# Optimization experiments

Hardware: AMD Instinct MI355X
Metric: run time of the kernel (lower is better)

Reference implementation:

```python
import jax, jax.numpy as jnp
import numpy as np

B, N, P, K, D = 8, 2048, 64, 32, 384
DEPTH, DI, DS, DCONV, DTR, NC = 12, 768, 16, 4, 24, 40
BN_EPS = 1e-5


def _spread_bits(v):
    v = v & 1023
    v = (v | (v << 16)) & 50331903
    v = (v | (v << 8)) & 50393103
    v = (v | (v << 4)) & 51130563
    v = (v | (v << 2)) & 153391689
    return v


def _zkey(x, y, z):
    return _spread_bits(x) | (_spread_bits(y) << 1) | (_spread_bits(z) << 2)


def _sfc_order(xyz, trans):
    lo = xyz.min(0, keepdims=True)
    hi = xyz.max(0, keepdims=True)
    q = jnp.clip(((xyz - lo) / (hi - lo + 1e-6) * 1023.0).astype(jnp.int32), 0, 1023)
    if trans:
        keys = _zkey(q[:, 2], q[:, 1], q[:, 0])
    else:
        keys = _zkey(q[:, 0], q[:, 1], q[:, 2])
    return jnp.argsort(keys)


def _ln(x, g, b):
    m = x.mean(-1, keepdims=True)
    v = jnp.var(x, axis=-1, keepdims=True)
    return (x - m) / jnp.sqrt(v + 1e-5) * g + b


def _bn_eval(x, g, b):
    # BatchNorm in eval mode, running_mean=0 / running_var=1
    return x * (g / np.float32(np.sqrt(1.0 + BN_EPS))) + b


def _patch_embed_one(xyz, w1, b1, g1, be1, w2, b2, g2, be2, w3, b3, g3, be3):
    # xyz: (N,3)
    cidx = (jnp.arange(P) * (N / P)).astype(jnp.int32)
    centers = xyz[cidx]                                      # (P,3)
    d2 = ((centers[:, None, :] - xyz[None, :, :]) ** 2).sum(-1)  # (P,N)
    _, knn = jax.lax.top_k(-d2, K)                           # (P,K) smallest dists
    nx = xyz[knn] - centers[:, None, :]                      # (P,K,3)
    h = jax.nn.gelu(_bn_eval(nx @ w1.T + b1, g1, be1), approximate=False)   # (P,K,64)
    h = jax.nn.gelu(_bn_eval(h @ w2.T + b2, g2, be2), approximate=False)    # (P,K,128)
    h = _bn_eval(h @ w3.T + b3, g3, be3)                     # (P,K,384)
    return h.max(1), centers


def _mamba(x, in_w, conv_w, conv_b, xp_w, dt_w, dt_b, Alog, Dp, out_w):
    # x: (B,L,D)
    Bsz, L, _ = x.shape
    xz = x @ in_w.T                                          # (B,L,2*DI)
    xc, z = xz[..., :DI], xz[..., DI:]
    xpad = jnp.pad(xc, ((0, 0), (DCONV - 1, 0), (0, 0)))
    xc = sum(xpad[:, j:j + L, :] * conv_w[:, j] for j in range(DCONV)) + conv_b
    xc = jax.nn.silu(xc)
    x_dbl = xc @ xp_w.T                                      # (B,L,DTR+2*DS)
    dt = x_dbl[..., :DTR]
    Bm = x_dbl[..., DTR:DTR + DS]
    Cm = x_dbl[..., DTR + DS:]
    delta = jax.nn.softplus(dt @ dt_w.T + dt_b)              # (B,L,DI)
    A = -jnp.exp(Alog)                                       # (DI,DS)

    def step(h, inp):
        d_t, B_t, C_t, u_t = inp                             # (B,DI),(B,DS),(B,DS),(B,DI)
        h = h * jnp.exp(d_t[..., None] * A) + (d_t * u_t)[..., None] * B_t[:, None, :]
        return h, jnp.einsum('bds,bs->bd', h, C_t)

    h0 = jnp.zeros((Bsz, DI, DS), x.dtype)
    inps = (delta.transpose(1, 0, 2), Bm.transpose(1, 0, 2),
            Cm.transpose(1, 0, 2), xc.transpose(1, 0, 2))
    _, ys = jax.lax.scan(step, h0, inps)                     # (L,B,DI)
    y = ys.transpose(1, 0, 2) + Dp * xc
    y = y * jax.nn.silu(z)
    return y @ out_w.T


def setup_inputs() -> dict:
    key = jax.random.key(0)
    ks = iter(jax.random.split(key, 64))
    nrm = lambda *s: jax.random.normal(next(ks), s, jnp.float32) * 0.02
    inp = {
        'data': jax.random.normal(next(ks), (B, N, 3), jnp.float32),
        'pe_w1': nrm(64, 3), 'pe_b1': jnp.zeros(64), 'pe_g1': jnp.ones(64), 'pe_be1': jnp.zeros(64),
        'pe_w2': nrm(128, 64), 'pe_b2': jnp.zeros(128), 'pe_g2': jnp.ones(128), 'pe_be2': jnp.zeros(128),
        'pe_w3': nrm(D, 128), 'pe_b3': jnp.zeros(D), 'pe_g3': jnp.ones(D), 'pe_be3': jnp.zeros(D),
        'oi_h_scale': jnp.ones(D), 'oi_h_shift': jnp.zeros(D),
        'oi_th_scale': jnp.ones(D), 'oi_th_shift': jnp.zeros(D),
        'pos_embed': nrm(1, P, D),
        'blk_ln_g': jnp.ones((DEPTH, D)), 'blk_ln_b': jnp.zeros((DEPTH, D)),
        'blk_in_w': nrm(DEPTH, 2 * DI, D),
        'blk_conv_w': nrm(DEPTH, DI, DCONV), 'blk_conv_b': jnp.zeros((DEPTH, DI)),
        'blk_xp_w': nrm(DEPTH, DTR + 2 * DS, DI),
        'blk_dt_w': nrm(DEPTH, DI, DTR), 'blk_dt_b': jnp.full((DEPTH, DI), -4.0),
        'blk_Alog': jnp.tile(jnp.log(jnp.arange(1, DS + 1, dtype=jnp.float32)), (DEPTH, DI, 1)),
        'blk_D': jnp.ones((DEPTH, DI)),
        'blk_out_w': nrm(DEPTH, D, DI),
        'norm_g': jnp.ones(D), 'norm_b': jnp.zeros(D),
        'mlp_w1': nrm(256, D), 'mlp_b1': jnp.zeros(256),
        'mlp_w2': nrm(64, 256), 'mlp_b2': jnp.zeros(64),
        'mlp_w3': nrm(NC, 64), 'mlp_b3': jnp.zeros(NC),
    }
    return inp


def reference(data, pe_w1, pe_b1, pe_g1, pe_be1, pe_w2, pe_b2, pe_g2, pe_be2,
              pe_w3, pe_b3, pe_g3, pe_be3, oi_h_scale, oi_h_shift, oi_th_scale,
              oi_th_shift, pos_embed, blk_ln_g, blk_ln_b, blk_in_w, blk_conv_w,
              blk_conv_b, blk_xp_w, blk_dt_w, blk_dt_b, blk_Alog, blk_D,
              blk_out_w, norm_g, norm_b, mlp_w1, mlp_b1, mlp_w2, mlp_b2,
              mlp_w3, mlp_b3):
    xyz = data[:, :, :3]
    tokens, centers = jax.vmap(
        _patch_embed_one, in_axes=(0,) + (None,) * 12)(
        xyz, pe_w1, pe_b1, pe_g1, pe_be1, pe_w2, pe_b2, pe_g2, pe_be2,
        pe_w3, pe_b3, pe_g3, pe_be3)                         # (B,P,D),(B,P,3)
    order_h = jax.vmap(lambda c: _sfc_order(c, False))(centers)
    order_th = jax.vmap(lambda c: _sfc_order(c, True))(centers)
    th = jnp.take_along_axis(tokens, order_h[:, :, None], axis=1) * oi_h_scale + oi_h_shift
    tth = jnp.take_along_axis(tokens, order_th[:, :, None], axis=1) * oi_th_scale + oi_th_shift
    t = jnp.concatenate([th + pos_embed, tth + pos_embed], axis=1)  # (B,2P,D)
    for i in range(DEPTH):
        t = t + _mamba(_ln(t, blk_ln_g[i], blk_ln_b[i]),
                       blk_in_w[i], blk_conv_w[i], blk_conv_b[i], blk_xp_w[i],
                       blk_dt_w[i], blk_dt_b[i], blk_Alog[i], blk_D[i], blk_out_w[i])
    t = _ln(t, norm_g, norm_b)
    x = t.mean(1)
    x = jax.nn.relu(x @ mlp_w1.T + mlp_b1)
    x = jax.nn.relu(x @ mlp_w2.T + mlp_b2)
    return x @ mlp_w3.T + mlp_b3
```

## Files before the change

kernel.cpp:

```cpp
#include <hip/hip_runtime.h>
#include <math.h>

#define BB 8
#define NN 2048
#define PP 64
#define KK 32
#define DD 384
#define DEPTH 12
#define DI 768
#define DS 16
#define DCONV 4
#define DTR 24
#define NC 40
#define LL 128
#define XROW (DTR + 2 * DS)
#define NR (BB * LL)

using bf16x8 = __attribute__((ext_vector_type(8))) short;
using floatx4 = __attribute__((ext_vector_type(4))) float;

__device__ __forceinline__ float gelu_exact(float x) {
    return 0.5f * x * (1.0f + erff(x * 0.70710678118654752440f));
}
__device__ __forceinline__ float siluf(float x) {
    return x / (1.0f + expf(-x));
}
__device__ __forceinline__ unsigned short f2bf(float f) {
    unsigned u = __float_as_uint(f);
    u += 0x7fffu + ((u >> 16) & 1u);
    return (unsigned short)(u >> 16);
}
__device__ __forceinline__ float bf2f(short s) {
    return __uint_as_float(((unsigned)(unsigned short)s) << 16);
}
__device__ __forceinline__ unsigned spread_bits(unsigned v) {
    v &= 1023u;
    v = (v | (v << 16)) & 50331903u;
    v = (v | (v << 8)) & 50393103u;
    v = (v | (v << 4)) & 51130563u;
    v = (v | (v << 2)) & 153391689u;
    return v;
}

__global__ void k_cvt(const float* __restrict__ in_w, const float* __restrict__ out_w,
                      const float* __restrict__ pe_w3, const float* __restrict__ xp,
                      const float* __restrict__ w2,
                      unsigned short* __restrict__ inwbf, unsigned short* __restrict__ owbf,
                      unsigned short* __restrict__ w3bf, unsigned short* __restrict__ xpbf,
                      unsigned short* __restrict__ w2bf)
{
    int idx = (blockIdx.x * 256 + threadIdx.x) * 4;
    const int n1 = DEPTH * 2 * DI * DD;
    const int n2 = DEPTH * DD * DI;
    const int n3 = DD * 128;
    const int n4 = DEPTH * 64 * DI;
    const int n5 = 128 * 64;
    if (idx < n1) {
        float4 v = *(const float4*)(in_w + idx);
        ushort4 o; o.x = f2bf(v.x); o.y = f2bf(v.y); o.z = f2bf(v.z); o.w = f2bf(v.w);
        *(ushort4*)(inwbf + idx) = o;
        return;
    }
    idx -= n1;
    if (idx < n2) {
        float4 v = *(const float4*)(out_w + idx);
        ushort4 o; o.x = f2bf(v.x); o.y = f2bf(v.y); o.z = f2bf(v.z); o.w = f2bf(v.w);
        *(ushort4*)(owbf + idx) = o;
        return;
    }
    idx -= n2;
    if (idx < n3) {
        float4 v = *(const float4*)(pe_w3 + idx);
        ushort4 o; o.x = f2bf(v.x); o.y = f2bf(v.y); o.z = f2bf(v.z); o.w = f2bf(v.w);
        *(ushort4*)(w3bf + idx) = o;
        return;
    }
    idx -= n3;
    if (idx < n4) {
        int i = idx / (64 * DI);
        int rem = idx - i * 64 * DI;
        int n = rem / DI, k = rem % DI;
        ushort4 o;
        if (n < XROW) {
            float4 v = *(const float4*)(xp + (size_t)i * XROW * DI + (size_t)n * DI + k);
            o.x = f2bf(v.x); o.y = f2bf(v.y); o.z = f2bf(v.z); o.w = f2bf(v.w);
        } else {
            o.x = o.y = o.z = o.w = 0;
        }
        *(ushort4*)(xpbf + (size_t)i * 64 * DI + (size_t)n * DI + k) = o;
        return;
    }
    idx -= n4;
    if (idx < n5) {
        float4 v = *(const float4*)(w2 + idx);
        ushort4 o; o.x = f2bf(v.x); o.y = f2bf(v.y); o.z = f2bf(v.z); o.w = f2bf(v.w);
        *(ushort4*)(w2bf + idx) = o;
    }
}

__global__ __launch_bounds__(256) void k_patch(
    const float* __restrict__ data,
    const float* __restrict__ w1, const float* __restrict__ b1,
    const float* __restrict__ g1, const float* __restrict__ be1,
    const unsigned short* __restrict__ w2bf, const float* __restrict__ b2,
    const float* __restrict__ g2, const float* __restrict__ be2,
    const unsigned short* __restrict__ w3bf, const float* __restrict__ b3,
    const float* __restrict__ g3, const float* __restrict__ be3,
    float* __restrict__ tokens, float* __restrict__ centers)
{
    const int bp = blockIdx.x;
    const int b = bp >> 6, p = bp & 63;
    const int tid = threadIdx.x;
    const float* X = data + (size_t)b * NN * 3;
    const float inv_den = 0.99999500003749968752f;

    __shared__ int hist[4][4][256];
    __shared__ int klist[KK];
    __shared__ int eqlist[256];
    __shared__ int s_kth, s_byte, s_cnt, s_eqcnt;
    __shared__ float nxs[KK * 3];
    __shared__ short h1b[KK][72];
    __shared__ short h2b[KK][136];

    const float cx = X[p * 32 * 3 + 0];
    const float cy = X[p * 32 * 3 + 1];
    const float cz = X[p * 32 * 3 + 2];
    if (tid == 0) {
        centers[(b * PP + p) * 3 + 0] = cx;
        centers[(b * PP + p) * 3 + 1] = cy;
        centers[(b * PP + p) * 3 + 2] = cz;
        s_kth = KK; s_cnt = 0; s_eqcnt = 0;
    }
    for (int i = tid; i < 4 * 4 * 256; i += 256) ((int*)hist)[i] = 0;

    const int wave = tid >> 6, lane = tid & 63;

    {
        unsigned key[8];
#pragma unroll
        for (int q = 0; q < 8; q++) {
            int i = tid + 256 * q;
            float dx = cx - X[i * 3 + 0];
            float dy = cy - X[i * 3 + 1];
            float dz = cz - X[i * 3 + 2];
            float d2 = dx * dx + dy * dy + dz * dz;
            key[q] = __float_as_uint(d2);
        }
        __syncthreads();
        unsigned prefix = 0;
        for (int rnd = 3; rnd >= 0; rnd--) {
            const int sh = rnd * 8;
            const int rslot = 3 - rnd;
            const unsigned pmask = (rnd == 3) ? 0u : (0xFFFFFFFFu << (8 * (rnd + 1)));
#pragma unroll
            for (int q = 0; q < 8; q++)
                if ((key[q] & pmask) == prefix)
                    atomicAdd(&hist[rslot][wave][(key[q] >> sh) & 255], 1);
            __syncthreads();
            if (wave == 0) {
                int c[4], tot = 0;
#pragma unroll
                for (int j = 0; j < 4; j++) {
                    int s4 = 0;
#pragma unroll
                    for (int w = 0; w < 4; w++) s4 += hist[rslot][w][lane * 4 + j];
                    c[j] = s4; tot += s4;
                }
                int inc = tot;
#pragma unroll
                for (int off = 1; off < 64; off <<= 1) {
                    int u = __shfl_up(inc, off);
                    if (lane >= off) inc += u;
                }
                int exc = inc - tot;
                int kth = s_kth;
                bool has = (exc < kth) && (exc + tot >= kth);
                unsigned long long bal = __ballot(has);
                int src = __ffsll(bal) - 1;
                if (lane == src) {
                    int rem = kth - exc;
                    int j = 0, cum = 0;
                    while (cum + c[j] < rem) { cum += c[j]; j++; }
                    s_byte = lane * 4 + j;
                    s_kth = rem - cum;
                }
            }
            __syncthreads();
            prefix |= ((unsigned)s_byte) << sh;
        }
        const unsigned kstar = prefix;
        const int need = s_kth;
#pragma unroll
        for (int q = 0; q < 8; q++) {
            int i = tid + 256 * q;
            if (key[q] < kstar) {
                int pos = atomicAdd(&s_cnt, 1);
                klist[pos] = i;
            } else if (key[q] == kstar) {
                int pos = atomicAdd(&s_eqcnt, 1);
                if (pos < 256) eqlist[pos] = i;
            }
        }
        __syncthreads();
        if (tid == 0) {
            int base = s_cnt;
            int ne = s_eqcnt < 256 ? s_eqcnt : 256;
            for (int k = 0; k < need; k++) {
                int best = 0x7fffffff, bi = 0;
                for (int j = 0; j < ne; j++)
                    if (eqlist[j] < best) { best = eqlist[j]; bi = j; }
                klist[base + k] = best;
                eqlist[bi] = 0x7fffffff;
            }
        }
        __syncthreads();
    }

    if (tid < KK) {
        int q = klist[tid];
        nxs[tid * 3 + 0] = X[q * 3 + 0] - cx;
        nxs[tid * 3 + 1] = X[q * 3 + 1] - cy;
        nxs[tid * 3 + 2] = X[q * 3 + 2] - cz;
    }
    __syncthreads();

    for (int e = tid; e < KK * 64; e += 256) {
        int j = e >> 6, c = e & 63;
        float v = nxs[j * 3 + 0] * w1[c * 3 + 0] + nxs[j * 3 + 1] * w1[c * 3 + 1] +
                  nxs[j * 3 + 2] * w1[c * 3 + 2] + b1[c];
        v = v * (g1[c] * inv_den) + be1[c];
        h1b[j][c] = (short)f2bf(gelu_exact(v));
    }
    __syncthreads();

    const int quad = lane >> 4, r = lane & 15;

    {
        floatx4 acc2[2][2] = {};
#pragma unroll
        for (int ks = 0; ks < 2; ks++) {
            const int k0 = ks * 32;
            bf16x8 af[2], bfv[2];
#pragma unroll
            for (int mi = 0; mi < 2; mi++)
                af[mi] = *(const bf16x8*)&h1b[mi * 16 + r][quad * 8 + k0];
#pragma unroll
            for (int jj = 0; jj < 2; jj++) {
                int n = wave * 32 + jj * 16 + r;
                bfv[jj] = *(const bf16x8*)(w2bf + (size_t)n * 64 + quad * 8 + k0);
            }
#pragma unroll
            for (int mi = 0; mi < 2; mi++)
#pragma unroll
                for (int jj = 0; jj < 2; jj++)
                    acc2[mi][jj] = __builtin_amdgcn_mfma_f32_16x16x32_bf16(af[mi], bfv[jj], acc2[mi][jj], 0, 0, 0);
        }
#pragma unroll
        for (int jj = 0; jj < 2; jj++) {
            int col = wave * 32 + jj * 16 + r;
            float sc = g2[col] * inv_den;
            float bb = b2[col] * sc + be2[col];
#pragma unroll
            for (int mi = 0; mi < 2; mi++)
#pragma unroll
                for (int r2 = 0; r2 < 4; r2++) {
                    int row = mi * 16 + quad * 4 + r2;
                    h2b[row][col] = (short)f2bf(gelu_exact(acc2[mi][jj][r2] * sc + bb));
                }
        }
    }
    __syncthreads();

    floatx4 acc3[2][6] = {};
#pragma unroll
    for (int ks = 0; ks < 4; ks++) {
        const int k0 = ks * 32;
        bf16x8 af[2];
        af[0] = *(const bf16x8*)&h2b[r][quad * 8 + k0];
        af[1] = *(const bf16x8*)&h2b[16 + r][quad * 8 + k0];
        bf16x8 bfv[6];
#pragma unroll
        for (int nj = 0; nj < 6; nj++) {
            int n = wave * 96 + nj * 16 + r;
            bfv[nj] = *(const bf16x8*)(w3bf + (size_t)n * 128 + quad * 8 + k0);
        }
#pragma unroll
        for (int mi = 0; mi < 2; mi++)
#pragma unroll
            for (int nj = 0; nj < 6; nj++)
                acc3[mi][nj] = __builtin_amdgcn_mfma_f32_16x16x32_bf16(af[mi], bfv[nj], acc3[mi][nj], 0, 0, 0);
    }
#pragma unroll
    for (int nj = 0; nj < 6; nj++) {
        int col = wave * 96 + nj * 16 + r;
        float sc = g3[col] * inv_den;
        float offc = b3[col] * sc + be3[col];
        float m = -3.4e38f;
#pragma unroll
        for (int mi = 0; mi < 2; mi++)
#pragma unroll
            for (int r2 = 0; r2 < 4; r2++)
                m = fmaxf(m, acc3[mi][nj][r2] * sc + offc);
        m = fmaxf(m, __shfl_xor(m, 16));
        m = fmaxf(m, __shfl_xor(m, 32));
        if (quad == 0) tokens[(size_t)bp * DD + col] = m;
    }
}

__global__ __launch_bounds__(256) void k_sfc_build(
    const float* __restrict__ centers, const float* __restrict__ tokens,
    const float* __restrict__ hs, const float* __restrict__ hb,
    const float* __restrict__ ts2, const float* __restrict__ tb2,
    const float* __restrict__ pos, float* __restrict__ tout)
{
    const int b = blockIdx.y, part = blockIdx.x;
    const int tid = threadIdx.x;

    __shared__ float csh[PP][3];
    __shared__ float slo[3], shi[3];
    __shared__ unsigned khs[PP], kts[PP];
    __shared__ int oh[PP], ot[PP];

    if (tid < PP) {
        csh[tid][0] = centers[(b * PP + tid) * 3 + 0];
        csh[tid][1] = centers[(b * PP + tid) * 3 + 1];
        csh[tid][2] = centers[(b * PP + tid) * 3 + 2];
    }
    __syncthreads();
    if (tid == 0) {
        for (int k = 0; k < 3; k++) {
            float lo = csh[0][k], hi = csh[0][k];
            for (int j = 1; j < PP; j++) { lo = fminf(lo, csh[j][k]); hi = fmaxf(hi, csh[j][k]); }
            slo[k] = lo; shi[k] = hi;
        }
    }
    __syncthreads();
    if (tid < PP) {
        int q[3];
        for (int k = 0; k < 3; k++) {
            float t = (csh[tid][k] - slo[k]) / (shi[k] - slo[k] + 1e-6f) * 1023.0f;
            int qi = (int)t;
            qi = qi < 0 ? 0 : (qi > 1023 ? 1023 : qi);
            q[k] = qi;
        }
        khs[tid] = spread_bits((unsigned)q[0]) | (spread_bits((unsigned)q[1]) << 1) |
                   (spread_bits((unsigned)q[2]) << 2);
        kts[tid] = spread_bits((unsigned)q[2]) | (spread_bits((unsigned)q[1]) << 1) |
                   (spread_bits((unsigned)q[0]) << 2);
    }
    __syncthreads();
    if (tid < PP) {
        unsigned kh = khs[tid], kt = kts[tid];
        int rh = 0, rt = 0;
        for (int j = 0; j < PP; j++) {
            unsigned a = khs[j];
            rh += (a < kh) || (a == kh && j < tid);
            unsigned c = kts[j];
            rt += (c < kt) || (c == kt && j < tid);
        }
        oh[rh] = tid;
        ot[rt] = tid;
    }
    __syncthreads();

    const int base = part * (LL * DD / 24);
    for (int e = tid; e < LL * DD / 24; e += 256) {
        int idx = base + e;
        int d = idx % DD;
        int l = idx / DD;
        float v;
        if (l < PP) {
            int src = oh[l];
            v = tokens[((size_t)b * PP + src) * DD + d] * hs[d] + hb[d] + pos[l * DD + d];
        } else {
            int l2 = l - PP;
            int src = ot[l2];
            v = tokens[((size_t)b * PP + src) * DD + d] * ts2[d] + tb2[d] + pos[l2 * DD + d];
        }
        tout[(size_t)b * LL * DD + idx] = v;
    }
}

__global__ __launch_bounds__(256) void k_stats(const float* __restrict__ t,
                                               const float* __restrict__ g,
                                               const float* __restrict__ gb,
                                               unsigned short* __restrict__ tbf,
                                               float* __restrict__ xdbl)
{
    const int tid = threadIdx.x;
    {
        int gi = blockIdx.x * 256 + tid;
        if (gi < NR * XROW) xdbl[gi] = 0.f;
    }
    const int wid = tid >> 6, lane = tid & 63;
    const int row = blockIdx.x * 4 + wid;
    const size_t base = (size_t)row * DD;
    float v[6];
    float s = 0.f, q = 0.f;
#pragma unroll
    for (int j = 0; j < 6; j++) {
        v[j] = t[base + lane + 64 * j];
        s += v[j]; q += v[j] * v[j];
    }
#pragma unroll
    for (int off = 32; off; off >>= 1) { s += __shfl_xor(s, off); q += __shfl_xor(q, off); }
    float mean = s * (1.0f / DD);
    float var = q * (1.0f / DD) - mean * mean;
    float inv = 1.0f / sqrtf(var + 1e-5f);
#pragma unroll
    for (int j = 0; j < 6; j++) {
        int i = lane + 64 * j;
        tbf[base + i] = f2bf((v[j] - mean) * inv * g[i] + gb[i]);
    }
}

__global__ __launch_bounds__(256) void k_mfma_xz(
    const unsigned short* __restrict__ tbf,
    const unsigned short* __restrict__ inwbf,
    const float* __restrict__ cw, const float* __restrict__ cb,
    const unsigned short* __restrict__ xpbf,
    unsigned short* __restrict__ xcbf, unsigned short* __restrict__ zsbf,
    float* __restrict__ xdbl)
{
    __shared__ short ct[128][72];
    const int tid = threadIdx.x;
    const int wave = tid >> 6, lane = tid & 63;
    const int quad = lane >> 4, r = lane & 15;
    const int wm = wave >> 1, wn = wave & 1;
    const int b = blockIdx.y;
    const int n0 = blockIdx.x * 64;
    const int m0 = b * 128 + wm * 64;

    floatx4 acc[4][2] = {};
    const unsigned short* Ab = tbf + (size_t)(m0 + r) * DD + quad * 8;
    const unsigned short* Bb = inwbf + (size_t)(n0 + wn * 32 + r) * DD + quad * 8;
    for (int k0 = 0; k0 < DD; k0 += 32) {
        bf16x8 af[4], bfv[2];
#pragma unroll
        for (int i = 0; i < 4; i++)
            af[i] = *(const bf16x8*)(Ab + (size_t)(i * 16) * DD + k0);
#pragma unroll
        for (int j = 0; j < 2; j++)
            bfv[j] = *(const bf16x8*)(Bb + (size_t)(j * 16) * DD + k0);
#pragma unroll
        for (int i = 0; i < 4; i++)
#pragma unroll
            for (int j = 0; j < 2; j++)
                acc[i][j] = __builtin_amdgcn_mfma_f32_16x16x32_bf16(af[i], bfv[j], acc[i][j], 0, 0, 0);
    }

#pragma unroll
    for (int i = 0; i < 4; i++)
#pragma unroll
        for (int r2 = 0; r2 < 4; r2++) {
            short* cp = &ct[wm * 64 + i * 16 + quad * 4 + r2][wn * 32 + r];
#pragma unroll
            for (int j = 0; j < 2; j++)
                cp[j * 16] = (short)f2bf(acc[i][j][r2]);
        }
    __syncthreads();

    const int l0 = (tid >> 3) * 4;
    const int c0 = (tid & 7) * 8;
    if (n0 < DI) {
        float cwv[8][4], cbv[8];
#pragma unroll
        for (int q = 0; q < 8; q++) {
            *(float4*)cwv[q] = *(const float4*)(cw + (size_t)(n0 + c0 + q) * 4);
            cbv[q] = cb[n0 + c0 + q];
        }
        unsigned short ov[4][8];
#pragma unroll
        for (int dl = 0; dl < 4; dl++) {
            const int l = l0 + dl;
            float u[8];
#pragma unroll
            for (int q = 0; q < 8; q++) u[q] = cbv[q];
#pragma unroll
            for (int j = 0; j < DCONV; j++) {
                int lt = l - (DCONV - 1) + j;
                if (lt >= 0) {
                    bf16x8 x = *(const bf16x8*)&ct[lt][c0];
#pragma unroll
                    for (int q = 0; q < 8; q++) u[q] += bf2f(x[q]) * cwv[q][j];
                }
            }
#pragma unroll
            for (int q = 0; q < 8; q++) ov[dl][q] = f2bf(siluf(u[q]));
        }
        __syncthreads();
#pragma unroll
        for (int dl = 0; dl < 4; dl++) {
            const int l = l0 + dl;
            *(bf16x8*)&ct[l][c0] = *(bf16x8*)ov[dl];
            *(bf16x8*)(xcbf + (size_t)(b * LL + l) * DI + n0 + c0) = *(bf16x8*)ov[dl];
        }
        __syncthreads();

        floatx4 acc2[2][4] = {};
#pragma unroll
        for (int k0 = 0; k0 < 64; k0 += 32) {
            bf16x8 af2[2], bfv2[4];
#pragma unroll
            for (int i = 0; i < 2; i++)
                af2[i] = *(const bf16x8*)&ct[wave * 32 + i * 16 + r][k0 + quad * 8];
#pragma unroll
            for (int nj = 0; nj < 4; nj++)
                bfv2[nj] = *(const bf16x8*)(xpbf + (size_t)(nj * 16 + r) * DI + n0 + k0 + quad * 8);
#pragma unroll
            for (int i = 0; i < 2; i++)
#pragma unroll
                for (int nj = 0; nj < 4; nj++)
                    acc2[i][nj] = __builtin_amdgcn_mfma_f32_16x16x32_bf16(af2[i], bfv2[nj], acc2[i][nj], 0, 0, 0);
        }
#pragma unroll
        for (int i = 0; i < 2; i++)
#pragma unroll
            for (int nj = 0; nj < 4; nj++) {
                int col = nj * 16 + r;
                if (col < XROW) {
#pragma unroll
                    for (int r2 = 0; r2 < 4; r2++) {
                        int row = b * LL + wave * 32 + i * 16 + quad * 4 + r2;
                        unsafeAtomicAdd(&xdbl[(size_t)row * XROW + col], acc2[i][nj][r2]);
                    }
                }
            }
    } else {
        const int nz = n0 - DI;
#pragma unroll
        for (int dl = 0; dl < 4; dl++) {
            const int l = l0 + dl;
            bf16x8 x = *(const bf16x8*)&ct[l][c0];
            unsigned short o[8];
#pragma unroll
            for (int q = 0; q < 8; q++) o[q] = f2bf(siluf(bf2f(x[q])));
            *(bf16x8*)(zsbf + (size_t)(b * LL + l) * DI + nz + c0) = *(bf16x8*)o;
        }
    }
}

__global__ __launch_bounds__(128) void k_scan(
    const float* __restrict__ xdbl,
    const unsigned short* __restrict__ xcbf, const unsigned short* __restrict__ zsbf,
    const float* __restrict__ dtw, const float* __restrict__ dtb,
    const float* __restrict__ Alog, const float* __restrict__ Dp,
    unsigned short* __restrict__ ybf)
{
    const int tid = threadIdx.x;
    const int b = blockIdx.x / DI;
    const int d = blockIdx.x % DI;

    __shared__ float sdel[LL];
    __shared__ float sdus[LL];
    __shared__ float sus[LL];
    __shared__ float szs[LL];
    __shared__ float negA[DS];
    __shared__ float ApL[DS][9];
    __shared__ float HlL[DS][9];
    __shared__ float hst[DS][9];

    {
        const int t = tid;
        const size_t row = (size_t)b * LL + t;
        const float* xd = xdbl + row * XROW;
        const float* w = dtw + d * DTR;
        float acc = dtb[d];
#pragma unroll
        for (int k = 0; k < DTR; k += 4) {
            float4 xv = *(const float4*)(xd + k);
            float4 wv = *(const float4*)(w + k);
            acc += xv.x * wv.x + xv.y * wv.y + xv.z * wv.z + xv.w * wv.w;
        }
        float delta = fmaxf(acc, 0.f) + log1pf(__expf(-fabsf(acc)));
        float u = bf2f((short)xcbf[row * DI + d]);
        sdel[t] = delta;
        sdus[t] = delta * u;
        sus[t] = u;
        szs[t] = bf2f((short)zsbf[row * DI + d]);
    }
    if (tid < DS) negA[tid] = -__expf(Alog[d * DS + tid]);
    __syncthreads();

    const int s = tid & 15;
    const int c = tid >> 4;
    const float* xB = xdbl + ((size_t)b * LL + c * 16) * XROW + DTR + s;

    float a_r[16], duB_r[16], C_r[16];
    {
        float h = 0.f, Ap = 1.f;
        const float na = negA[s];
#pragma unroll
        for (int q = 0; q < 16; q++) {
            int t = c * 16 + q;
            float a = __expf(sdel[t] * na);
            float Bv = xB[(size_t)q * XROW];
            float Cv = xB[(size_t)q * XROW + DS];
            a_r[q] = a;
            duB_r[q] = sdus[t] * Bv;
            C_r[q] = Cv;
            h = h * a + duB_r[q];
            Ap *= a;
        }
        ApL[s][c] = Ap;
        HlL[s][c] = h;
    }
    __syncthreads();
    if (tid < DS) {
        float hs = 0.f;
#pragma unroll
        for (int cc = 0; cc < 8; cc++) {
            hst[tid][cc] = hs;
            hs = ApL[tid][cc] * hs + HlL[tid][cc];
        }
    }
    __syncthreads();

    {
        const float Dd = Dp[d];
        float h = hst[s][c];
        unsigned short* yc = ybf + ((size_t)b * LL + c * 16) * DI + d;
#pragma unroll
        for (int q = 0; q < 16; q++) {
            h = h * a_r[q] + duB_r[q];
            float p = h * C_r[q];
            p += __shfl_xor(p, 1, 16);
            p += __shfl_xor(p, 2, 16);
            p += __shfl_xor(p, 4, 16);
            p += __shfl_xor(p, 8, 16);
            if (s == 0) {
                int t = c * 16 + q;
                yc[(size_t)q * DI] = f2bf((p + Dd * sus[t]) * szs[t]);
            }
        }
    }
}

__global__ __launch_bounds__(256) void k_mfma_op(
    const unsigned short* __restrict__ ybf,
    const unsigned short* __restrict__ owbf,
    float* __restrict__ t)
{
    const int tid = threadIdx.x;
    const int wave = tid >> 6, lane = tid & 63;
    const int quad = lane >> 4, r = lane & 15;
    const int wr2 = wave >> 1, wc = wave & 1;
    const int n0 = blockIdx.x * 64 + wc * 32;
    const int m0 = blockIdx.y * 32 + wr2 * 16;
    const int kb = blockIdx.z * (DI / 2);

    floatx4 acc[2] = {};
    const unsigned short* Ab = ybf + (size_t)(m0 + r) * DI + kb + quad * 8;
    const unsigned short* Bb = owbf + (size_t)(n0 + r) * DI + kb + quad * 8;
    for (int k0 = 0; k0 < DI / 2; k0 += 32) {
        bf16x8 af = *(const bf16x8*)(Ab + k0);
        bf16x8 b0 = *(const bf16x8*)(Bb + k0);
        bf16x8 b1 = *(const bf16x8*)(Bb + (size_t)16 * DI + k0);
        acc[0] = __builtin_amdgcn_mfma_f32_16x16x32_bf16(af, b0, acc[0], 0, 0, 0);
        acc[1] = __builtin_amdgcn_mfma_f32_16x16x32_bf16(af, b1, acc[1], 0, 0, 0);
    }

#pragma unroll
    for (int j = 0; j < 2; j++) {
        int col = n0 + j * 16 + r;
#pragma unroll
        for (int r2 = 0; r2 < 4; r2++) {
            int row = m0 + quad * 4 + r2;
            unsafeAtomicAdd(t + (size_t)row * DD + col, acc[j][r2]);
        }
    }
}

__global__ __launch_bounds__(256) void k_lnpool(const float* __restrict__ t,
                                                const float* __restrict__ ng,
                                                const float* __restrict__ nb,
                                                float* __restrict__ pparts)
{
    const int b = blockIdx.y, chunk = blockIdx.x;
    const int tid = threadIdx.x;
    const int wave = tid >> 6, lane = tid & 63;
    __shared__ float pw[4][DD];

    for (int c = lane; c < DD; c += 64) pw[wave][c] = 0.f;
    __syncthreads();

    for (int rr = 0; rr < 4; rr++) {
        const int row = b * LL + chunk * 16 + wave * 4 + rr;
        const float* xr = t + (size_t)row * DD;
        float v[6];
        float s = 0.f, q = 0.f;
#pragma unroll
        for (int j = 0; j < 6; j++) { v[j] = xr[lane + 64 * j]; s += v[j]; q += v[j] * v[j]; }
#pragma unroll
        for (int off = 32; off; off >>= 1) { s += __shfl_xor(s, off); q += __shfl_xor(q, off); }
        float mean = s * (1.0f / DD);
        float var = q * (1.0f / DD) - mean * mean;
        float inv = 1.0f / sqrtf(var + 1e-5f);
#pragma unroll
        for (int j = 0; j < 6; j++) {
            int c = lane + 64 * j;
            pw[wave][c] += (v[j] - mean) * inv * ng[c] + nb[c];
        }
    }
    __syncthreads();
    float* out = pparts + ((size_t)b * 8 + chunk) * DD;
    for (int c = tid; c < DD; c += 256)
        out[c] = pw[0][c] + pw[1][c] + pw[2][c] + pw[3][c];
}

__global__ __launch_bounds__(256) void k_mlp(const float* __restrict__ pparts,
    const float* __restrict__ w1, const float* __restrict__ b1,
    const float* __restrict__ w2, const float* __restrict__ b2,
    const float* __restrict__ w3, const float* __restrict__ b3,
    float* __restrict__ out)
{
    const int b = blockIdx.x, tid = threadIdx.x;
    __shared__ float pl[DD];
    __shared__ float h1[256];
    __shared__ float h2[64];
    for (int c = tid; c < DD; c += 256) {
        const float* pp = pparts + (size_t)b * 8 * DD + c;
        float s = 0.f;
#pragma unroll
        for (int z = 0; z < 8; z++) s += pp[z * DD];
        pl[c] = s * (1.0f / LL);
    }
    __syncthreads();

    {
        float acc = b1[tid];
        const float* wr = w1 + (size_t)tid * DD;
        for (int k = 0; k < DD; k++) acc += pl[k] * wr[k];
        h1[tid] = fmaxf(acc, 0.f);
    }
    __syncthreads();
    if (tid < 64) {
        float acc = b2[tid];
        const float* wr = w2 + (size_t)tid * 256;
        for (int k = 0; k < 256; k++) acc += h1[k] * wr[k];
        h2[tid] = fmaxf(acc, 0.f);
    }
    __syncthreads();
    if (tid < NC) {
        float acc = b3[tid];
        const float* wr = w3 + (size_t)tid * 64;
        for (int k = 0; k < 64; k++) acc += h2[k] * wr[k];
        out[b * NC + tid] = acc;
    }
}

extern "C" void kernel_launch(void* const* d_in, const int* in_sizes, int n_in,
                              void* d_out, int out_size, void* d_ws, size_t ws_size,
                              hipStream_t stream)
{
    const float* data      = (const float*)d_in[0];
    const float* pe_w1     = (const float*)d_in[1];
    const float* pe_b1     = (const float*)d_in[2];
    const float* pe_g1     = (const float*)d_in[3];
    const float* pe_be1    = (const float*)d_in[4];
    const float* pe_w2     = (const float*)d_in[5];
    const float* pe_b2     = (const float*)d_in[6];
    const float* pe_g2     = (const float*)d_in[7];
    const float* pe_be2    = (const float*)d_in[8];
    const float* pe_w3     = (const float*)d_in[9];
    const float* pe_b3     = (const float*)d_in[10];
    const float* pe_g3     = (const float*)d_in[11];
    const float* pe_be3    = (const float*)d_in[12];
    const float* oi_h_scale  = (const float*)d_in[13];
    const float* oi_h_shift  = (const float*)d_in[14];
    const float* oi_th_scale = (const float*)d_in[15];
    const float* oi_th_shift = (const float*)d_in[16];
    const float* pos_embed = (const float*)d_in[17];
    const float* blk_ln_g  = (const float*)d_in[18];
    const float* blk_ln_b  = (const float*)d_in[19];
    const float* blk_in_w  = (const float*)d_in[20];
    const float* blk_conv_w = (const float*)d_in[21];
    const float* blk_conv_b = (const float*)d_in[22];
    const float* blk_xp_w  = (const float*)d_in[23];
    const float* blk_dt_w  = (const float*)d_in[24];
    const float* blk_dt_b  = (const float*)d_in[25];
    const float* blk_Alog  = (const float*)d_in[26];
    const float* blk_D     = (const float*)d_in[27];
    const float* blk_out_w = (const float*)d_in[28];
    const float* norm_g    = (const float*)d_in[29];
    const float* norm_b    = (const float*)d_in[30];
    const float* mlp_w1    = (const float*)d_in[31];
    const float* mlp_b1    = (const float*)d_in[32];
    const float* mlp_w2    = (const float*)d_in[33];
    const float* mlp_b2    = (const float*)d_in[34];
    const float* mlp_w3    = (const float*)d_in[35];
    const float* mlp_b3    = (const float*)d_in[36];

    float* ws = (float*)d_ws;
    size_t off = 0;
    auto alloc = [&](size_t n) { float* p = ws + off; off += (n + 63) & ~(size_t)63; return p; };
    float* tokens  = alloc((size_t)BB * PP * DD);
    float* centers = alloc((size_t)BB * PP * 3);
    float* t    = alloc((size_t)NR * DD);
    float* xdbl = alloc((size_t)NR * XROW);
    float* pparts  = alloc((size_t)BB * 8 * DD);
    unsigned short* tbf   = (unsigned short*)alloc((size_t)NR * DD / 2);
    unsigned short* xcbf  = (unsigned short*)alloc((size_t)NR * DI / 2);
    unsigned short* zsbf  = (unsigned short*)alloc((size_t)NR * DI / 2);
    unsigned short* ybf   = (unsigned short*)alloc((size_t)NR * DI / 2);
    unsigned short* inwbf = (unsigned short*)alloc((size_t)DEPTH * 2 * DI * DD / 2);
    unsigned short* owbf  = (unsigned short*)alloc((size_t)DEPTH * DD * DI / 2);
    unsigned short* xpbf  = (unsigned short*)alloc((size_t)DEPTH * 64 * DI / 2);
    unsigned short* w3bf  = (unsigned short*)alloc((size_t)DD * 128 / 2);
    unsigned short* w2bf  = (unsigned short*)alloc((size_t)128 * 64 / 2);

    {
        const int total = DEPTH * 2 * DI * DD + DEPTH * DD * DI + DD * 128 + DEPTH * 64 * DI + 128 * 64;
        k_cvt<<<(total / 4 + 255) / 256, 256, 0, stream>>>(
            blk_in_w, blk_out_w, pe_w3, blk_xp_w, pe_w2, inwbf, owbf, w3bf, xpbf, w2bf);
    }

    k_patch<<<BB * PP, 256, 0, stream>>>(data,
        pe_w1, pe_b1, pe_g1, pe_be1, w2bf, pe_b2, pe_g2, pe_be2,
        w3bf, pe_b3, pe_g3, pe_be3, tokens, centers);
    k_sfc_build<<<dim3(24, BB), 256, 0, stream>>>(centers, tokens,
        oi_h_scale, oi_h_shift, oi_th_scale, oi_th_shift, pos_embed, t);

    for (int i = 0; i < DEPTH; i++) {
        const float* ln_g = blk_ln_g + i * DD;
        const float* ln_b = blk_ln_b + i * DD;
        const float* cw   = blk_conv_w + (size_t)i * DI * DCONV;
        const float* cb   = blk_conv_b + (size_t)i * DI;
        const float* dtw  = blk_dt_w + (size_t)i * DI * DTR;
        const float* dtb  = blk_dt_b + (size_t)i * DI;
        const float* Al   = blk_Alog + (size_t)i * DI * DS;
        const float* Dpp  = blk_D + (size_t)i * DI;
        const unsigned short* inw = inwbf + (size_t)i * 2 * DI * DD;
        const unsigned short* ow  = owbf + (size_t)i * DD * DI;
        const unsigned short* xpb = xpbf + (size_t)i * 64 * DI;

        k_stats<<<NR / 4, 256, 0, stream>>>(t, ln_g, ln_b, tbf, xdbl);
        k_mfma_xz<<<dim3(24, BB), 256, 0, stream>>>(
            tbf, inw, cw, cb, xpb, xcbf, zsbf, xdbl);
        k_scan<<<BB * DI, 128, 0, stream>>>(xdbl, xcbf, zsbf, dtw, dtb, Al, Dpp, ybf);
        k_mfma_op<<<dim3(DD / 64, NR / 32, 2), 256, 0, stream>>>(ybf, ow, t);
    }

    k_lnpool<<<dim3(8, BB), 256, 0, stream>>>(t, norm_g, norm_b, pparts);
    k_mlp<<<BB, 256, 0, stream>>>(pparts, mlp_w1, mlp_b1, mlp_w2, mlp_b2, mlp_w3, mlp_b3,
                                  (float*)d_out);
}
```

Baseline: 915.1 us.

## Fuse LayerNorm into in-projection GEMM and relocate xdbl zeroing

Drops the separate per-layer LayerNorm kernel. Each in-projection block now computes row statistics, normalizes its 128 rows to bf16 in LDS in two K-halves, and feeds the MFMA from LDS instead of a global bf16 buffer. The xdbl accumulator zeroing moves to the SFC build kernel for the first layer and to the out-projection kernel for later layers. This removes 12 launches and one global round-trip of the normalized activations. In exchange every column block recomputes the LayerNorm of the same rows redundantly, and the larger LDS footprint may lower occupancy.

```diff
diff --git a/kernel.cpp b/kernel.cpp
--- a/kernel.cpp
+++ b/kernel.cpp
@@ -311,10 +311,16 @@
     const float* __restrict__ centers, const float* __restrict__ tokens,
     const float* __restrict__ hs, const float* __restrict__ hb,
     const float* __restrict__ ts2, const float* __restrict__ tb2,
-    const float* __restrict__ pos, float* __restrict__ tout)
+    const float* __restrict__ pos, float* __restrict__ tout,
+    float* __restrict__ xd0)
 {
     const int b = blockIdx.y, part = blockIdx.x;
     const int tid = threadIdx.x;
+
+    {
+        int fid = (b * 24 + part) * 256 + tid;
+        for (int i = fid; i < NR * XROW; i += 24 * BB * 256) xd0[i] = 0.f;
+    }
 
     __shared__ float csh[PP][3];
     __shared__ float slo[3], shi[3];
@@ -381,72 +387,87 @@
     }
 }
 
-__global__ __launch_bounds__(256) void k_stats(const float* __restrict__ t,
-                                               const float* __restrict__ g,
-                                               const float* __restrict__ gb,
-                                               unsigned short* __restrict__ tbf,
-                                               float* __restrict__ xdbl)
-{
-    const int tid = threadIdx.x;
-    {
-        int gi = blockIdx.x * 256 + tid;
-        if (gi < NR * XROW) xdbl[gi] = 0.f;
-    }
-    const int wid = tid >> 6, lane = tid & 63;
-    const int row = blockIdx.x * 4 + wid;
-    const size_t base = (size_t)row * DD;
-    float v[6];
-    float s = 0.f, q = 0.f;
-#pragma unroll
-    for (int j = 0; j < 6; j++) {
-        v[j] = t[base + lane + 64 * j];
-        s += v[j]; q += v[j] * v[j];
-    }
-#pragma unroll
-    for (int off = 32; off; off >>= 1) { s += __shfl_xor(s, off); q += __shfl_xor(q, off); }
-    float mean = s * (1.0f / DD);
-    float var = q * (1.0f / DD) - mean * mean;
-    float inv = 1.0f / sqrtf(var + 1e-5f);
-#pragma unroll
-    for (int j = 0; j < 6; j++) {
-        int i = lane + 64 * j;
-        tbf[base + i] = f2bf((v[j] - mean) * inv * g[i] + gb[i]);
-    }
-}
-
 __global__ __launch_bounds__(256) void k_mfma_xz(
-    const unsigned short* __restrict__ tbf,
+    const float* __restrict__ t,
+    const float* __restrict__ ln_g, const float* __restrict__ ln_b,
     const unsigned short* __restrict__ inwbf,
     const float* __restrict__ cw, const float* __restrict__ cb,
     const unsigned short* __restrict__ xpbf,
     unsigned short* __restrict__ xcbf, unsigned short* __restrict__ zsbf,
     float* __restrict__ xdbl)
 {
-    __shared__ short ct[128][72];
+    __shared__ float smean[128], sinv[128];
+    __shared__ short lnA[128][200];
+    short (*ct)[72] = (short (*)[72])&lnA[0][0];
+
     const int tid = threadIdx.x;
     const int wave = tid >> 6, lane = tid & 63;
     const int quad = lane >> 4, r = lane & 15;
     const int wm = wave >> 1, wn = wave & 1;
     const int b = blockIdx.y;
     const int n0 = blockIdx.x * 64;
-    const int m0 = b * 128 + wm * 64;
+
+    {
+        const int row = tid >> 1, seg = tid & 1;
+        const float* xr = t + (size_t)(b * LL + row) * DD + seg * 4;
+        float s = 0.f, q = 0.f;
+#pragma unroll
+        for (int i = 0; i < 48; i++) {
+            float4 v = *(const float4*)(xr + i * 8);
+            s += v.x + v.y + v.z + v.w;
+            q += v.x * v.x + v.y * v.y + v.z * v.z + v.w * v.w;
+        }
+        s += __shfl_xor(s, 1);
+        q += __shfl_xor(q, 1);
+        if (seg == 0) {
+            float mean = s * (1.0f / DD);
+            float var = q * (1.0f / DD) - mean * mean;
+            smean[row] = mean;
+            sinv[row] = 1.0f / sqrtf(var + 1e-5f);
+        }
+    }
+    __syncthreads();
 
     floatx4 acc[4][2] = {};
-    const unsigned short* Ab = tbf + (size_t)(m0 + r) * DD + quad * 8;
-    const unsigned short* Bb = inwbf + (size_t)(n0 + wn * 32 + r) * DD + quad * 8;
-    for (int k0 = 0; k0 < DD; k0 += 32) {
-        bf16x8 af[4], bfv[2];
-#pragma unroll
-        for (int i = 0; i < 4; i++)
-            af[i] = *(const bf16x8*)(Ab + (size_t)(i * 16) * DD + k0);
-#pragma unroll
-        for (int j = 0; j < 2; j++)
-            bfv[j] = *(const bf16x8*)(Bb + (size_t)(j * 16) * DD + k0);
-#pragma unroll
-        for (int i = 0; i < 4; i++)
+    for (int kh = 0; kh < 2; kh++) {
+        {
+            const int row = tid >> 1;
+            const int cb0 = (tid & 1) * 96;
+            const float mean = smean[row];
+            const float inv = sinv[row];
+            const float* xr = t + (size_t)(b * LL + row) * DD + kh * 192 + cb0;
+            const float* gg = ln_g + kh * 192 + cb0;
+            const float* bb = ln_b + kh * 192 + cb0;
+#pragma unroll
+            for (int i = 0; i < 24; i++) {
+                float4 v = *(const float4*)(xr + i * 4);
+                float4 g4 = *(const float4*)(gg + i * 4);
+                float4 b4 = *(const float4*)(bb + i * 4);
+                ushort4 o;
+                o.x = f2bf((v.x - mean) * inv * g4.x + b4.x);
+                o.y = f2bf((v.y - mean) * inv * g4.y + b4.y);
+                o.z = f2bf((v.z - mean) * inv * g4.z + b4.z);
+                o.w = f2bf((v.w - mean) * inv * g4.w + b4.w);
+                *(ushort4*)&lnA[row][cb0 + i * 4] = o;
+            }
+        }
+        __syncthreads();
+        const unsigned short* Bb = inwbf + (size_t)(n0 + wn * 32 + r) * DD + kh * 192 + quad * 8;
+        for (int k0 = 0; k0 < 192; k0 += 32) {
+            bf16x8 af[4], bfv[2];
+#pragma unroll
+            for (int i = 0; i < 4; i++)
+                af[i] = *(const bf16x8*)&lnA[wm * 64 + i * 16 + r][k0 + quad * 8];
 #pragma unroll
             for (int j = 0; j < 2; j++)
-                acc[i][j] = __builtin_amdgcn_mfma_f32_16x16x32_bf16(af[i], bfv[j], acc[i][j], 0, 0, 0);
+                bfv[j] = *(const bf16x8*)(Bb + (size_t)(j * 16) * DD + k0);
+#pragma unroll
+            for (int i = 0; i < 4; i++)
+#pragma unroll
+                for (int j = 0; j < 2; j++)
+                    acc[i][j] = __builtin_amdgcn_mfma_f32_16x16x32_bf16(af[i], bfv[j], acc[i][j], 0, 0, 0);
+        }
+        __syncthreads();
     }
 
 #pragma unroll
@@ -639,9 +660,13 @@
 __global__ __launch_bounds__(256) void k_mfma_op(
     const unsigned short* __restrict__ ybf,
     const unsigned short* __restrict__ owbf,
-    float* __restrict__ t)
+    float* __restrict__ t, float* __restrict__ xdbl)
 {
     const int tid = threadIdx.x;
+    {
+        int gi = ((blockIdx.z * 32 + blockIdx.y) * 6 + blockIdx.x) * 256 + tid;
+        if (gi < NR * XROW) xdbl[gi] = 0.f;
+    }
     const int wave = tid >> 6, lane = tid & 63;
     const int quad = lane >> 4, r = lane & 15;
     const int wr2 = wave >> 1, wc = wave & 1;
@@ -799,7 +824,6 @@
     float* t    = alloc((size_t)NR * DD);
     float* xdbl = alloc((size_t)NR * XROW);
     float* pparts  = alloc((size_t)BB * 8 * DD);
-    unsigned short* tbf   = (unsigned short*)alloc((size_t)NR * DD / 2);
     unsigned short* xcbf  = (unsigned short*)alloc((size_t)NR * DI / 2);
     unsigned short* zsbf  = (unsigned short*)alloc((size_t)NR * DI / 2);
     unsigned short* ybf   = (unsigned short*)alloc((size_t)NR * DI / 2);
@@ -819,7 +843,7 @@
         pe_w1, pe_b1, pe_g1, pe_be1, w2bf, pe_b2, pe_g2, pe_be2,
         w3bf, pe_b3, pe_g3, pe_be3, tokens, centers);
     k_sfc_build<<<dim3(24, BB), 256, 0, stream>>>(centers, tokens,
-        oi_h_scale, oi_h_shift, oi_th_scale, oi_th_shift, pos_embed, t);
+        oi_h_scale, oi_h_shift, oi_th_scale, oi_th_shift, pos_embed, t, xdbl);
 
     for (int i = 0; i < DEPTH; i++) {
         const float* ln_g = blk_ln_g + i * DD;
@@ -834,11 +858,10 @@
         const unsigned short* ow  = owbf + (size_t)i * DD * DI;
         const unsigned short* xpb = xpbf + (size_t)i * 64 * DI;
 
-        k_stats<<<NR / 4, 256, 0, stream>>>(t, ln_g, ln_b, tbf, xdbl);
         k_mfma_xz<<<dim3(24, BB), 256, 0, stream>>>(
-            tbf, inw, cw, cb, xpb, xcbf, zsbf, xdbl);
+            t, ln_g, ln_b, inw, cw, cb, xpb, xcbf, zsbf, xdbl);
         k_scan<<<BB * DI, 128, 0, stream>>>(xdbl, xcbf, zsbf, dtw, dtb, Al, Dpp, ybf);
-        k_mfma_op<<<dim3(DD / 64, NR / 32, 2), 256, 0, stream>>>(ybf, ow, t);
+        k_mfma_op<<<dim3(DD / 64, NR / 32, 2), 256, 0, stream>>>(ybf, ow, t, xdbl);
     }
 
     k_lnpool<<<dim3(8, BB), 256, 0, stream>>>(t, norm_g, norm_b, pparts);
```

After: 999.3 us. 9.2% more time.
